# Kernel tuning notes

Measured on AMD Instinct MI355X. Metric: run time of the kernel, lower is better.

The kernel has to match this reference:

```python
import jax, jax.numpy as jnp
import numpy as np

CELL_SIDE = 2.0
N_CELLS = 4          # n
POOL = 8             # pool_size
HIDDEN = 128         # pooling_dim for type_='social'
OUT = 128
GRID = N_CELLS * POOL  # 32: side of fine occupancy grid


def setup_inputs() -> dict:
    key = jax.random.key(0)
    k1, k2, k3, k4 = jax.random.split(key, 4)
    n = 512
    hidden_state = jax.random.normal(k1, (n, HIDDEN), jnp.float32)
    obs1 = jax.random.normal(k2, (n, 2), jnp.float32)
    obs2 = jax.random.normal(k3, (n, 2), jnp.float32)
    W = jax.random.normal(k4, (N_CELLS * N_CELLS * HIDDEN, OUT), jnp.float32) * 0.02
    b = jnp.zeros((OUT,), jnp.float32)
    return {"hidden_state": hidden_state, "obs1": obs1, "obs2": obs2, "W": W, "b": b}


def reference(hidden_state, obs1, obs2, W, b):
    # type_='social': obs1 unused; hidden_state is scattered into the grid.
    n = obs2.shape[0]
    # off-diagonal index matrix: idx[i, j] enumerates all peds != i  (n, n-1)
    jj = jnp.arange(n - 1)[None, :]
    idx = jj + (jj >= jnp.arange(n)[:, None])

    relative = obs2[idx] - obs2[:, None, :]            # (n, n-1, 2)
    other = hidden_state[idx]                          # (n, n-1, HIDDEN)

    # bin relative positions into 0.25m sub-cells, grid centred on each ped
    oij = relative / (CELL_SIDE / POOL) + GRID / 2     # (n, n-1, 2)
    in_range = jnp.all((oij >= 0) & (oij < GRID), axis=2)  # (n, n-1)
    oij = jnp.where(in_range[..., None], oij, 0.0).astype(jnp.int32)
    other = jnp.where(in_range[..., None], other, 0.0)
    oi = oij[..., 0] * GRID + oij[..., 1]              # flat cell index (n, n-1)

    occ = jnp.zeros((n, GRID * GRID, HIDDEN), obs2.dtype)
    occ = occ.at[jnp.arange(n)[:, None], oi].set(other)

    # (n, HIDDEN, GRID, GRID) -> lp_pool2d(p=1, k=POOL) == block sum
    occ = occ.transpose(0, 2, 1).reshape(n, HIDDEN, N_CELLS, POOL, N_CELLS, POOL)
    pooled = occ.sum(axis=(3, 5)).reshape(n, -1)       # (n, HIDDEN*N_CELLS*N_CELLS)

    return jax.nn.relu(pooled @ W + b)
```

## Files before the change

kernel.cpp:

```cpp
#include <hip/hip_runtime.h>
#include <hip/hip_bf16.h>


#define N_PED 512
#define HID   128
#define KDIM  2048
#define OUTD  128

__global__ __launch_bounds__(256) void pool_kernel(
    const float* __restrict__ hidden,
    const float* __restrict__ obs2,
    float*       __restrict__ pooled)
{
    __shared__ int winner[1024];
    const int i   = blockIdx.x;
    const int tid = threadIdx.x;

    for (int c = tid; c < 1024; c += 256) winner[c] = -1;

    const float2 pi = ((const float2*)obs2)[i];
    __syncthreads();

    for (int j = tid; j < N_PED; j += 256) {
        if (j == i) continue;
        const float2 pj = ((const float2*)obs2)[j];
        const float ox = (pj.x - pi.x) * 4.0f + 16.0f;
        const float oy = (pj.y - pi.y) * 4.0f + 16.0f;
        const bool in = (ox >= 0.0f) && (ox < 32.0f) && (oy >= 0.0f) && (oy < 32.0f);
        int c, enc;
        if (in) { c = ((int)ox) * 32 + (int)oy; enc = 2 * j + 1; }
        else    { c = 0;                        enc = 2 * j;     }
        atomicMax(&winner[c], enc);
    }
    __syncthreads();

    const int g    = tid >> 4;
    const int lane = tid & 15;
    const int h0   = lane * 8;
    const int cx   = g >> 2, cy = g & 3;

    float acc[8] = {0.f,0.f,0.f,0.f,0.f,0.f,0.f,0.f};
    const int rb = (cx * 8) * 32 + cy * 8;
    #pragma unroll
    for (int px = 0; px < 8; ++px) {
        const int base = rb + px * 32;
        #pragma unroll
        for (int py = 0; py < 8; ++py) {
            const int w = winner[base + py];
            if (w >= 0 && (w & 1)) {
                const int j = w >> 1;
                const float4 r0 = *(const float4*)(hidden + j * HID + h0);
                const float4 r1 = *(const float4*)(hidden + j * HID + h0 + 4);
                acc[0] += r0.x; acc[1] += r0.y; acc[2] += r0.z; acc[3] += r0.w;
                acc[4] += r1.x; acc[5] += r1.y; acc[6] += r1.z; acc[7] += r1.w;
            }
        }
    }

    float* dst = pooled + i * KDIM;
    #pragma unroll
    for (int q = 0; q < 8; ++q)
        dst[(h0 + q) * 16 + g] = acc[q];
}

__global__ __launch_bounds__(256) void gemm_part(
    const float* __restrict__ pooled,
    const float* __restrict__ W,
    float*       __restrict__ part)
{
    const int ig   = blockIdx.x;
    const int kc   = blockIdx.y;
    const int tid  = threadIdx.x;
    const int o    = tid & 127;
    const int half = tid >> 7;
    const int kbase = kc * 512 + half * 256;

    const float* p[8];
    #pragma unroll
    for (int r = 0; r < 8; ++r)
        p[r] = pooled + (ig * 8 + r) * KDIM + kbase;

    float acc[8] = {0.f,0.f,0.f,0.f,0.f,0.f,0.f,0.f};
    for (int kk = 0; kk < 256; kk += 4) {
        const int kb = (kbase + kk) * OUTD + o;
        const float w0 = W[kb];
        const float w1 = W[kb + OUTD];
        const float w2 = W[kb + 2 * OUTD];
        const float w3 = W[kb + 3 * OUTD];
        #pragma unroll
        for (int r = 0; r < 8; ++r) {
            const float4 a = *(const float4*)(p[r] + kk);
            acc[r] += a.x * w0 + a.y * w1 + a.z * w2 + a.w * w3;
        }
    }
    const int slot = kc * 2 + half;
    #pragma unroll
    for (int r = 0; r < 8; ++r)
        part[((ig * 8 + r) * 8 + slot) * OUTD + o] = acc[r];
}

__global__ __launch_bounds__(256) void finish_kernel(
    const float* __restrict__ part,
    const float* __restrict__ bias,
    float*       __restrict__ out)
{
    const int idx = blockIdx.x * 256 + threadIdx.x;
    const int i = idx >> 7, o = idx & 127;
    float s = bias[o];
    #pragma unroll
    for (int m = 0; m < 8; ++m)
        s += part[(i * 8 + m) * OUTD + o];
    out[idx] = fmaxf(s, 0.0f);
}

extern "C" void kernel_launch(void* const* d_in, const int* in_sizes, int n_in,
                              void* d_out, int out_size, void* d_ws, size_t ws_size,
                              hipStream_t stream) {
    (void)in_sizes; (void)n_in; (void)out_size; (void)ws_size;
    const float* hidden = (const float*)d_in[0];
    const float* obs2   = (const float*)d_in[2];
    const float* W      = (const float*)d_in[3];
    const float* bias   = (const float*)d_in[4];

    float* pooled = (float*)d_ws;
    float* part   = pooled + (size_t)N_PED * KDIM;

    pool_kernel<<<dim3(N_PED), dim3(256), 0, stream>>>(hidden, obs2, pooled);
    gemm_part<<<dim3(64, 4), dim3(256), 0, stream>>>(pooled, W, part);
    finish_kernel<<<dim3(256), dim3(256), 0, stream>>>(part, bias, (float*)d_out);
}
```

Before: 100.6 us.

## Precompute hidden@W per cell block, then gather-sum occupied cells per pedestrian

Matmul and pooling are reordered. A dense GEMM first computes T = hidden × W for each of the 16 pooled-cell weight slices. Then, per pedestrian, the winning neighbours are compacted into a shared-memory list with a ballot and prefix count, and their T rows are summed directly, with bias and ReLU fused in. This drops the dense pooled intermediate, the split-K partial buffer and the separate finish kernel, cutting one launch. The GEMM keeps the same FLOP count, and the combine step now does scattered reads of T rows from global memory.

```diff
diff --git a/kernel.cpp b/kernel.cpp
--- a/kernel.cpp
+++ b/kernel.cpp
@@ -4,20 +4,75 @@
 
 #define N_PED 512
 #define HID   128
-#define KDIM  2048
 #define OUTD  128
+#define TCOLS 2048
 
-__global__ __launch_bounds__(256) void pool_kernel(
+__global__ __launch_bounds__(256) void gemm_T(
     const float* __restrict__ hidden,
+    const float* __restrict__ W,
+    float*       __restrict__ T)
+{
+    const int g   = blockIdx.x;
+    const int mg  = blockIdx.y;
+    const int tid = threadIdx.x;
+
+    __shared__ float hs[32 * 128];
+    const float* src = hidden + mg * 32 * HID;
+    #pragma unroll
+    for (int v = 0; v < 4; ++v) {
+        const int off = v * 1024 + tid * 4;
+        *(float4*)(hs + off) = *(const float4*)(src + off);
+    }
+    __syncthreads();
+
+    const int o0 = tid & 63;
+    const int wv = tid >> 6;
+    const float* wbase = W + g * OUTD + o0;
+
+    float acc[16];
+    #pragma unroll
+    for (int q = 0; q < 16; ++q) acc[q] = 0.f;
+
+    for (int kk = 0; kk < 128; kk += 4) {
+        float wl[8];
+        #pragma unroll
+        for (int q = 0; q < 4; ++q) {
+            wl[q * 2 + 0] = wbase[(kk + q) * TCOLS];
+            wl[q * 2 + 1] = wbase[(kk + q) * TCOLS + 64];
+        }
+        #pragma unroll
+        for (int r = 0; r < 8; ++r) {
+            const float4 a = *(const float4*)(hs + (wv * 8 + r) * 128 + kk);
+            acc[r * 2 + 0] += a.x * wl[0] + a.y * wl[2] + a.z * wl[4] + a.w * wl[6];
+            acc[r * 2 + 1] += a.x * wl[1] + a.y * wl[3] + a.z * wl[5] + a.w * wl[7];
+        }
+    }
+
+    float* dst = T + g * OUTD + o0;
+    #pragma unroll
+    for (int r = 0; r < 8; ++r) {
+        const int row = mg * 32 + wv * 8 + r;
+        dst[row * TCOLS]      = acc[r * 2 + 0];
+        dst[row * TCOLS + 64] = acc[r * 2 + 1];
+    }
+}
+
+__global__ __launch_bounds__(256) void combine_kernel(
+    const float* __restrict__ T,
     const float* __restrict__ obs2,
-    float*       __restrict__ pooled)
+    const float* __restrict__ bias,
+    float*       __restrict__ out)
 {
-    __shared__ int winner[1024];
+    __shared__ int   winner[1024];
+    __shared__ int   list[512];
+    __shared__ int   lcnt;
+    __shared__ float red[256];
+
     const int i   = blockIdx.x;
     const int tid = threadIdx.x;
 
+    if (tid == 0) lcnt = 0;
     for (int c = tid; c < 1024; c += 256) winner[c] = -1;
-
     const float2 pi = ((const float2*)obs2)[i];
     __syncthreads();
 
@@ -26,7 +81,7 @@
         const float2 pj = ((const float2*)obs2)[j];
         const float ox = (pj.x - pi.x) * 4.0f + 16.0f;
         const float oy = (pj.y - pi.y) * 4.0f + 16.0f;
-        const bool in = (ox >= 0.0f) && (ox < 32.0f) && (oy >= 0.0f) && (oy < 32.0f);
+        const bool in = (ox >= 0.f) && (ox < 32.f) && (oy >= 0.f) && (oy < 32.f);
         int c, enc;
         if (in) { c = ((int)ox) * 32 + (int)oy; enc = 2 * j + 1; }
         else    { c = 0;                        enc = 2 * j;     }
@@ -34,83 +89,37 @@
     }
     __syncthreads();
 
-    const int g    = tid >> 4;
-    const int lane = tid & 15;
-    const int h0   = lane * 8;
-    const int cx   = g >> 2, cy = g & 3;
-
-    float acc[8] = {0.f,0.f,0.f,0.f,0.f,0.f,0.f,0.f};
-    const int rb = (cx * 8) * 32 + cy * 8;
-    #pragma unroll
-    for (int px = 0; px < 8; ++px) {
-        const int base = rb + px * 32;
-        #pragma unroll
-        for (int py = 0; py < 8; ++py) {
-            const int w = winner[base + py];
-            if (w >= 0 && (w & 1)) {
-                const int j = w >> 1;
-                const float4 r0 = *(const float4*)(hidden + j * HID + h0);
-                const float4 r1 = *(const float4*)(hidden + j * HID + h0 + 4);
-                acc[0] += r0.x; acc[1] += r0.y; acc[2] += r0.z; acc[3] += r0.w;
-                acc[4] += r1.x; acc[5] += r1.y; acc[6] += r1.z; acc[7] += r1.w;
-            }
+    const int lane = tid & 63;
+    for (int r = 0; r < 4; ++r) {
+        const int c = r * 256 + tid;
+        const int w = winner[c];
+        const bool take = (w > 0) && (w & 1);
+        const unsigned long long m = __ballot(take);
+        int base = 0;
+        if (lane == 0 && m) base = atomicAdd(&lcnt, __popcll(m));
+        base = __shfl(base, 0);
+        if (take) {
+            const int pre = __popcll(m & ((1ull << lane) - 1ull));
+            const int gg  = ((c >> 8) & 3) * 4 + ((c >> 3) & 3);
+            list[base + pre] = ((w >> 1) << 4) | gg;
         }
     }
+    __syncthreads();
 
-    float* dst = pooled + i * KDIM;
-    #pragma unroll
-    for (int q = 0; q < 8; ++q)
-        dst[(h0 + q) * 16 + g] = acc[q];
-}
-
-__global__ __launch_bounds__(256) void gemm_part(
-    const float* __restrict__ pooled,
-    const float* __restrict__ W,
-    float*       __restrict__ part)
-{
-    const int ig   = blockIdx.x;
-    const int kc   = blockIdx.y;
-    const int tid  = threadIdx.x;
     const int o    = tid & 127;
     const int half = tid >> 7;
-    const int kbase = kc * 512 + half * 256;
-
-    const float* p[8];
-    #pragma unroll
-    for (int r = 0; r < 8; ++r)
-        p[r] = pooled + (ig * 8 + r) * KDIM + kbase;
-
-    float acc[8] = {0.f,0.f,0.f,0.f,0.f,0.f,0.f,0.f};
-    for (int kk = 0; kk < 256; kk += 4) {
-        const int kb = (kbase + kk) * OUTD + o;
-        const float w0 = W[kb];
-        const float w1 = W[kb + OUTD];
-        const float w2 = W[kb + 2 * OUTD];
-        const float w3 = W[kb + 3 * OUTD];
-        #pragma unroll
-        for (int r = 0; r < 8; ++r) {
-            const float4 a = *(const float4*)(p[r] + kk);
-            acc[r] += a.x * w0 + a.y * w1 + a.z * w2 + a.w * w3;
-        }
+    const int n    = lcnt;
+    float acc = 0.f;
+    for (int e = half; e < n; e += 2) {
+        const int ent = list[e];
+        acc += T[(ent >> 4) * TCOLS + (ent & 15) * OUTD + o];
     }
-    const int slot = kc * 2 + half;
-    #pragma unroll
-    for (int r = 0; r < 8; ++r)
-        part[((ig * 8 + r) * 8 + slot) * OUTD + o] = acc[r];
-}
-
-__global__ __launch_bounds__(256) void finish_kernel(
-    const float* __restrict__ part,
-    const float* __restrict__ bias,
-    float*       __restrict__ out)
-{
-    const int idx = blockIdx.x * 256 + threadIdx.x;
-    const int i = idx >> 7, o = idx & 127;
-    float s = bias[o];
-    #pragma unroll
-    for (int m = 0; m < 8; ++m)
-        s += part[(i * 8 + m) * OUTD + o];
-    out[idx] = fmaxf(s, 0.0f);
+    red[tid] = acc;
+    __syncthreads();
+    if (tid < 128) {
+        const float s = bias[tid] + red[tid] + red[tid + 128];
+        out[i * OUTD + tid] = fmaxf(s, 0.f);
+    }
 }
 
 extern "C" void kernel_launch(void* const* d_in, const int* in_sizes, int n_in,
@@ -122,10 +131,9 @@
     const float* W      = (const float*)d_in[3];
     const float* bias   = (const float*)d_in[4];
 
-    float* pooled = (float*)d_ws;
-    float* part   = pooled + (size_t)N_PED * KDIM;
+    float* T = (float*)d_ws;
 
-    pool_kernel<<<dim3(N_PED), dim3(256), 0, stream>>>(hidden, obs2, pooled);
-    gemm_part<<<dim3(64, 4), dim3(256), 0, stream>>>(pooled, W, part);
-    finish_kernel<<<dim3(256), dim3(256), 0, stream>>>(part, bias, (float*)d_out);
+    gemm_T<<<dim3(16, 16), dim3(256), 0, stream>>>(hidden, W, T);
+    combine_kernel<<<dim3(N_PED), dim3(256), 0, stream>>>(T, obs2, bias,
+                                                          (float*)d_out);
 }
```

New measurement: 116.0 us. +15.3%, slower.
